# Kernel optimization log

Hardware: AMD Instinct MI355X
Metric: run time of the kernel (lower is better)

## Reference

```python
import jax, jax.numpy as jnp
import numpy as np

BN_EPS = 1e-5
TEMPERATURE = 256 ** 0.5  # sqrt(c2), since cv3 = ScaledDotProductAttention(c2)


def conv_bn_silu(x, w, gamma, beta, mean, var):
    # Conv2d(k=3, s=1, pad='same', bias=False) -> BatchNorm2d (running stats) -> SiLU
    y = jax.lax.conv_general_dilated(
        x, w, window_strides=(1, 1), padding='SAME',
        dimension_numbers=('NCHW', 'OIHW', 'NCHW'))
    scale = (gamma / jnp.sqrt(var + BN_EPS))[None, :, None, None]
    shift = (beta - mean * gamma / jnp.sqrt(var + BN_EPS))[None, :, None, None]
    y = y * scale + shift
    return y * jax.nn.sigmoid(y)  # SiLU


def setup_inputs() -> dict:
    key = jax.random.key(0)
    ks = jax.random.split(key, 8)
    B, C, H, W = 16, 256, 64, 64
    Ch = 128  # hidden channels c_ = int(c2 * e)
    x = jax.random.normal(ks[0], (B, C, H, W), dtype=jnp.float32)
    w1 = jax.random.normal(ks[1], (Ch, C, 3, 3), dtype=jnp.float32) * 0.05
    g1 = jnp.ones((Ch,), jnp.float32) + 0.1 * jax.random.normal(ks[2], (Ch,), dtype=jnp.float32)
    b1 = 0.1 * jax.random.normal(ks[3], (Ch,), dtype=jnp.float32)
    m1 = 0.1 * jax.random.normal(ks[4], (Ch,), dtype=jnp.float32)
    v1 = jnp.ones((Ch,), jnp.float32) + 0.5 * jax.random.uniform(ks[5], (Ch,), dtype=jnp.float32)
    w2 = jax.random.normal(ks[6], (C, Ch, 3, 3), dtype=jnp.float32) * 0.05
    g2 = jnp.ones((C,), jnp.float32)
    b2 = jnp.zeros((C,), jnp.float32)
    m2 = 0.1 * jax.random.normal(ks[7], (C,), dtype=jnp.float32)
    v2 = jnp.ones((C,), jnp.float32) + 0.5 * jax.random.uniform(jax.random.fold_in(key, 99), (C,), dtype=jnp.float32)
    return {"x": x, "w1": w1, "g1": g1, "b1": b1, "m1": m1, "v1": v1,
            "w2": w2, "g2": g2, "b2": b2, "m2": m2, "v2": v2}


def reference(x, w1, g1, b1, m1, v1, w2, g2, b2, m2, v2):
    y = conv_bn_silu(x, w1, g1, b1, m1, v1)       # [B, 128, H, W]
    y = conv_bn_silu(y, w2, g2, b2, m2, v2)       # [B, 256, H, W]
    B, C, H, W = y.shape
    q = y.reshape(B, C, H * W)                    # q = k^T = v, all views of y
    # channel-channel attention: scores [B, C, C]
    scores = jnp.einsum('bcn,bdn->bcd', q / TEMPERATURE, q)
    attn = jax.nn.softmax(scores, axis=-1)        # dropout is identity in eval
    out = jnp.einsum('bcd,bdn->bcn', attn, q).reshape(B, C, H, W)
    return x + out  # shortcut: c1 == c2
```

## Files before the change

kernel.cpp:

```cpp
#include <hip/hip_runtime.h>
#include <math.h>

#define BB 16
#define C1 256
#define CHD 128
#define NN 4096
#define INV_T (1.0f/16.0f)

typedef _Float16 half8 __attribute__((ext_vector_type(8)));
typedef __attribute__((ext_vector_type(4))) float f32x4;
typedef __attribute__((ext_vector_type(16))) float f32x16;

__device__ inline unsigned short f2h(float f) {
    _Float16 h = (_Float16)f;
    return __builtin_bit_cast(unsigned short, h);
}

#define GLDS(g, l) __builtin_amdgcn_global_load_lds(                              \
    (const __attribute__((address_space(1))) unsigned int*)(g),                   \
    (__attribute__((address_space(3))) unsigned int*)(l), 16, 0, 0)

__global__ __launch_bounds__(256) void nchw_to_nhwc_f16(
    const float* __restrict__ x, unsigned short* __restrict__ xh, int C)
{
    const int c0 = blockIdx.x * 64;
    const int hp = blockIdx.y;
    const int b  = blockIdx.z;
    const int nCk = C >> 4;

    if (hp == 0 || hp == 65) {
        for (int idx = threadIdx.x; idx < 1024; idx += 256) {
            int w = idx >> 4, cq = (idx & 15) * 4;
            ushort4 z; z.x = z.y = z.z = z.w = 0;
            *(ushort4*)&xh[((((size_t)b * nCk + (c0 >> 4) + (cq >> 4)) * 66 + hp) * 64 + w) * 16
                           + (cq & 15)] = z;
        }
        return;
    }
    const int h = hp - 1;
    __shared__ float ts[64][65];
    for (int idx = threadIdx.x; idx < 4096; idx += 256) {
        int cl = idx >> 6, w = idx & 63;
        ts[cl][w] = x[(((size_t)b * C + c0 + cl) * 64 + h) * 64 + w];
    }
    __syncthreads();
    for (int idx = threadIdx.x; idx < 1024; idx += 256) {
        int w = idx >> 4, cq = (idx & 15) * 4;
        ushort4 o;
        o.x = f2h(ts[cq + 0][w]); o.y = f2h(ts[cq + 1][w]);
        o.z = f2h(ts[cq + 2][w]); o.w = f2h(ts[cq + 3][w]);
        *(ushort4*)&xh[((((size_t)b * nCk + (c0 >> 4) + (cq >> 4)) * 66 + hp) * 64 + w) * 16
                       + (cq & 15)] = o;
    }
}

__global__ __launch_bounds__(256) void pack_w_kernel(
    const float* __restrict__ w, unsigned short* __restrict__ wT, int Cout, int Cin)
{
    int idx = blockIdx.x * 256 + threadIdx.x;
    int total = Cout * Cin * 9;
    if (idx >= total) return;
    int ci = idx % Cin; int t = idx / Cin; int co = t % Cout; int kk = t / Cout;
    wT[((((size_t)(ci >> 4)) * 9 + kk) * Cout + co) * 16 + (ci & 15)] =
        f2h(w[((size_t)co * Cin + ci) * 9 + kk]);
}

__global__ __launch_bounds__(256) void zero_y1h_pads(unsigned short* __restrict__ y1h)
{
    int idx = blockIdx.x * 256 + threadIdx.x;
    int b   = idx >> 12;
    int ck  = (idx >> 9) & 7;
    int row = ((idx >> 8) & 1) ? 65 : 0;
    int w   = (idx >> 2) & 63;
    int qtr = idx & 3;
    ushort4 z; z.x = z.y = z.z = z.w = 0;
    *(ushort4*)&y1h[((((size_t)b * 8 + ck) * 66 + row) * 64 + w) * 16 + qtr * 4] = z;
}

__global__ __launch_bounds__(512, 4) void conv_mfma_kernel(
    const unsigned short* __restrict__ xh, const unsigned short* __restrict__ wT,
    const float* __restrict__ gamma, const float* __restrict__ beta,
    const float* __restrict__ mean, const float* __restrict__ var,
    unsigned short* __restrict__ outNHWC,
    unsigned short* __restrict__ yhi, unsigned short* __restrict__ yhiT,
    int Cin, int Cout)
{
    const int tid  = threadIdx.x;
    const int wid  = tid >> 6;
    const int lane = tid & 63;
    const int l31  = lane & 31;
    const int hi   = lane >> 5;
    const int coBase = blockIdx.x * 64;
    const int h0     = blockIdx.y * 8;
    const int b      = blockIdx.z;
    const int nCk    = Cin >> 4;

    __shared__ __align__(16) unsigned short smem[39552];
    __shared__ float bnsc[64], bnsh[64];

    if (tid < 64) {
        int co = coBase + tid;
        float sc = gamma[co] * rsqrtf(var[co] + 1e-5f);
        bnsc[tid] = sc;
        bnsh[tid] = beta[co] - mean[co] * sc;
    }
    if (tid < 160) {
        int cell = tid >> 2;
        int part = tid & 3;
        int buf  = cell & 1;
        int col  = ((cell >> 1) & 1) ? 65 : 0;
        int r    = cell >> 2;
        ushort4 z; z.x = z.y = z.z = z.w = 0;
        *(ushort4*)&smem[buf * 10560 + (r * 66 + col) * 16 + part * 4] = z;
    }

    auto stage = [&](int sel, int ck) {
        unsigned short* wsd = smem + 21120 + sel * 9216;
        unsigned short* xsd = smem + sel * 10560;
        for (int it = wid; it < 38; it += 8) {
            if (it < 18) {
                int kk = it >> 1, h = it & 1;
                const unsigned short* g =
                    wT + (((size_t)ck * 9 + kk) * Cout + coBase + h * 32) * 16 + lane * 8;
                GLDS(g, wsd + (kk * 64 + h * 32) * 16);
            } else {
                int j = it - 18;
                int r = j >> 1, hf = j & 1;
                const unsigned short* g =
                    xh + ((((size_t)b * nCk + ck) * 66 + h0 + r) * 64 + hf * 32) * 16 + lane * 8;
                GLDS(g, xsd + (r * 66 + 1 + hf * 32) * 16);
            }
        }
    };

    stage(0, 0);
    __syncthreads();

    f32x16 acc[2][2] = {};

    int sel = 0;
    for (int ck = 0; ck < nCk; ck++) {
        if (ck + 1 < nCk) stage(sel ^ 1, ck + 1);

        const unsigned short* wsb = smem + 21120 + sel * 9216;
        const unsigned short* xsb = smem + sel * 10560;
#pragma unroll
        for (int kk = 0; kk < 9; kk++) {
            const int kh = kk / 3, kw = kk % 3;
            half8 a0 = *(const half8*)&wsb[(kk * 64 +      l31) * 16 + hi * 8];
            half8 a1 = *(const half8*)&wsb[(kk * 64 + 32 + l31) * 16 + hi * 8];
            const unsigned short* xr = &xsb[((wid + kh) * 66 + l31 + kw) * 16 + hi * 8];
            half8 b0 = *(const half8*)xr;
            half8 b1 = *(const half8*)&xr[32 * 16];
            acc[0][0] = __builtin_amdgcn_mfma_f32_32x32x16_f16(a0, b0, acc[0][0], 0, 0, 0);
            acc[0][1] = __builtin_amdgcn_mfma_f32_32x32x16_f16(a0, b1, acc[0][1], 0, 0, 0);
            acc[1][0] = __builtin_amdgcn_mfma_f32_32x32x16_f16(a1, b0, acc[1][0], 0, 0, 0);
            acc[1][1] = __builtin_amdgcn_mfma_f32_32x32x16_f16(a1, b1, acc[1][1], 0, 0, 0);
        }
        __syncthreads();
        sel ^= 1;
    }

    const int orow = h0 + wid;
    const bool isConv1 = (outNHWC != nullptr);

    __syncthreads();

#pragma unroll
    for (int mi = 0; mi < 2; mi++)
#pragma unroll
        for (int ni = 0; ni < 2; ni++) {
            f32x16 a = acc[mi][ni];
            int w = ni * 32 + l31;
            int swz = ((l31 + wid) & 7) << 3;
#pragma unroll
            for (int rq = 0; rq < 4; rq++) {
                int c0 = mi * 32 + rq * 8 + hi * 4;
                ushort4 o; unsigned short* op = (unsigned short*)&o;
#pragma unroll
                for (int r = 0; r < 4; r++) {
                    float t = a[rq * 4 + r] * bnsc[c0 + r] + bnsh[c0 + r];
                    float s = t / (1.f + __expf(-t));
                    op[r] = f2h(s);
                    if (!isConv1)
                        yhi[(((size_t)b * Cout + coBase + c0 + r) * 64 + orow) * 64 + w] = op[r];
                }
                *(ushort4*)&smem[wid * 4096 + w * 64 + (c0 ^ swz)] = o;
            }
        }
    __syncthreads();

    const int ckB = blockIdx.x * 4;
    const int nCkOut = Cout >> 4;
#pragma unroll
    for (int j = 0; j < 8; j++) {
        int g   = j * 512 + tid;
        int s   = g & 1;
        int w   = (g >> 1) & 63;
        int row = (g >> 7) & 7;
        int ck  = g >> 10;
        uint4 v = *(const uint4*)&smem[row * 4096 + w * 64 +
                     (((ck * 2 + s) * 8) ^ (((w + row) & 7) << 3))];
        if (isConv1) {
            *(uint4*)&outNHWC[((((size_t)b * nCkOut + ckB + ck) * 66 + h0 + row + 1) * 64 + w) * 16
                              + s * 8] = v;
        } else {
            *(uint4*)&yhiT[(((size_t)b * nCkOut + ckB + ck) * 4096 + (size_t)(h0 + row) * 64 + w) * 16
                           + s * 8] = v;
        }
    }
}

__global__ __launch_bounds__(256) void scores_mfma_kernel(
    const unsigned short* __restrict__ yhi, float* __restrict__ scores)
{
    static const int TI[10] = {0,0,0,0,1,1,1,2,2,3};
    static const int TJ[10] = {0,1,2,3,1,2,3,2,3,3};
    const int b  = blockIdx.z;
    const int ti = TI[blockIdx.x], tj = TJ[blockIdx.x];
    const int cB = ti * 64;
    const int dB = tj * 64;
    const int tid  = threadIdx.x;
    const int wid  = tid >> 6;
    const int lane = tid & 63;
    const int ln   = lane & 15;
    const int q    = lane >> 4;
    const int wm   = wid >> 1, wn = wid & 1;

    __shared__ unsigned short As[64 * 128];
    __shared__ unsigned short Bs[64 * 128];

    const int rl = lane >> 4;
    const int gl = lane & 15;

    f32x4 acc[2][2] = {};

    for (int ck = 0; ck < 32; ck++) {
        const int n0 = ck * 128;
        for (int it = wid; it < 32; it += 4) {
            const int tile = it >> 4;
            const int j = it & 15;
            const int r = j * 4 + rl;
            const int gq = gl ^ (r & 7);
            const int rowAbs = (tile ? dB : cB) + r;
            const unsigned short* g =
                yhi + ((size_t)b * 256 + rowAbs) * 4096 + n0 + gq * 8;
            GLDS(g, (tile ? Bs : As) + j * 512);
        }
        __syncthreads();

#pragma unroll
        for (int kwin = 0; kwin < 4; kwin++) {
            half8 ah[2], bh[2];
#pragma unroll
            for (int mi = 0; mi < 2; mi++) {
                int row = wm * 32 + mi * 16 + ln;
                ah[mi] = *(const half8*)&As[row * 128 + ((kwin * 4 + q) ^ (ln & 7)) * 8];
            }
#pragma unroll
            for (int ni = 0; ni < 2; ni++) {
                int row = wn * 32 + ni * 16 + ln;
                bh[ni] = *(const half8*)&Bs[row * 128 + ((kwin * 4 + q) ^ (ln & 7)) * 8];
            }
#pragma unroll
            for (int mi = 0; mi < 2; mi++)
#pragma unroll
                for (int ni = 0; ni < 2; ni++)
                    acc[mi][ni] = __builtin_amdgcn_mfma_f32_16x16x32_f16(
                        ah[mi], bh[ni], acc[mi][ni], 0, 0, 0);
        }
        __syncthreads();
    }

#pragma unroll
    for (int mi = 0; mi < 2; mi++)
#pragma unroll
        for (int ni = 0; ni < 2; ni++) {
            f32x4 a = acc[mi][ni];
            float vals[4];
            vals[0] = a.x * INV_T; vals[1] = a.y * INV_T;
            vals[2] = a.z * INV_T; vals[3] = a.w * INV_T;
            int c0 = cB + wm * 32 + mi * 16 + q * 4;
            int d  = dB + wn * 32 + ni * 16 + ln;
#pragma unroll
            for (int r = 0; r < 4; r++)
                scores[((size_t)b * C1 + c0 + r) * C1 + d] = vals[r];
            if (ti != tj) {
                float4 tv = {vals[0], vals[1], vals[2], vals[3]};
                *(float4*)&scores[((size_t)b * C1 + d) * C1 + c0] = tv;
            }
        }
}

__global__ __launch_bounds__(64) void softmax_kernel(
    const float* __restrict__ scores, unsigned short* __restrict__ attn16)
{
    const int row = blockIdx.x;
    const float* p = scores + (size_t)row * C1;
    const int lane = threadIdx.x;

    float4 v = ((const float4*)p)[lane];
    float m = fmaxf(fmaxf(v.x, v.y), fmaxf(v.z, v.w));
#pragma unroll
    for (int off = 32; off >= 1; off >>= 1)
        m = fmaxf(m, __shfl_xor(m, off, 64));

    float4 e;
    e.x = expf(v.x - m); e.y = expf(v.y - m);
    e.z = expf(v.z - m); e.w = expf(v.w - m);
    float s = e.x + e.y + e.z + e.w;
#pragma unroll
    for (int off = 32; off >= 1; off >>= 1)
        s += __shfl_xor(s, off, 64);
    float inv = 1.f / s;
    ushort4 o;
    o.x = f2h(e.x * inv); o.y = f2h(e.y * inv);
    o.z = f2h(e.z * inv); o.w = f2h(e.w * inv);
    *(ushort4*)&attn16[(size_t)row * C1 + lane * 4] = o;
}

__global__ __launch_bounds__(256) void out_mfma_kernel(
    const unsigned short* __restrict__ attn16, const unsigned short* __restrict__ yhiT,
    const float* __restrict__ x, float* __restrict__ out)
{
    const int b  = blockIdx.z;
    const int cB = blockIdx.y * 64;
    const int nB = blockIdx.x * 128;
    const int tid  = threadIdx.x;
    const int wid  = tid >> 6;
    const int lane = tid & 63;
    const int ln   = lane & 15;
    const int q    = lane >> 4;
    const int wm   = wid >> 1, wn = wid & 1;

    __shared__ unsigned short As[64 * 64];
    __shared__ unsigned short Bs[4 * 128 * 16];

    const int r8 = lane >> 3;
    const int gq = (lane & 7) ^ r8;

    f32x4 acc[2][4] = {};

    for (int ck = 0; ck < 4; ck++) {
        const int d0 = ck * 64;
        for (int it = wid; it < 24; it += 4) {
            if (it < 8) {
                const unsigned short* g =
                    attn16 + ((size_t)b * 256 + cB + it * 8 + r8) * 256 + d0 + gq * 8;
                GLDS(g, As + it * 512);
            } else {
                int j = it - 8;
                int u = j >> 2, part = j & 3;
                const unsigned short* g =
                    yhiT + (((size_t)b * 16 + ck * 4 + u) * 4096 + nB + part * 32) * 16 + lane * 8;
                GLDS(g, Bs + (u * 128 + part * 32) * 16);
            }
        }
        __syncthreads();

#pragma unroll
        for (int kwin = 0; kwin < 2; kwin++) {
            const int cc = (((kwin * 4 + q) ^ (ln & 7))) * 8;
            const int gK = kwin * 4 + q;
            half8 af[2], bfr[4];
#pragma unroll
            for (int mi = 0; mi < 2; mi++)
                af[mi] = *(const half8*)&As[(wm * 32 + mi * 16 + ln) * 64 + cc];
#pragma unroll
            for (int ni = 0; ni < 4; ni++) {
                int row = wn * 64 + ni * 16 + ln;
                bfr[ni] = *(const half8*)&Bs[(gK >> 1) * 2048 + row * 16 + (gK & 1) * 8];
            }
#pragma unroll
            for (int mi = 0; mi < 2; mi++)
#pragma unroll
                for (int ni = 0; ni < 4; ni++)
                    acc[mi][ni] = __builtin_amdgcn_mfma_f32_16x16x32_f16(
                        af[mi], bfr[ni], acc[mi][ni], 0, 0, 0);
        }
        __syncthreads();
    }

#pragma unroll
    for (int mi = 0; mi < 2; mi++)
#pragma unroll
        for (int ni = 0; ni < 4; ni++) {
            f32x4 a = acc[mi][ni];
            float vals[4] = {a.x, a.y, a.z, a.w};
#pragma unroll
            for (int r = 0; r < 4; r++) {
                int c = cB + wm * 32 + mi * 16 + q * 4 + r;
                int n = nB + wn * 64 + ni * 16 + ln;
                size_t o = ((size_t)b * C1 + c) * NN + n;
                out[o] = x[o] + vals[r];
            }
        }
}

extern "C" void kernel_launch(void* const* d_in, const int* in_sizes, int n_in,
                              void* d_out, int out_size, void* d_ws, size_t ws_size,
                              hipStream_t stream)
{
    const float* x  = (const float*)d_in[0];
    const float* w1 = (const float*)d_in[1];
    const float* g1 = (const float*)d_in[2];
    const float* b1 = (const float*)d_in[3];
    const float* m1 = (const float*)d_in[4];
    const float* v1 = (const float*)d_in[5];
    const float* w2 = (const float*)d_in[6];
    const float* g2 = (const float*)d_in[7];
    const float* b2 = (const float*)d_in[8];
    const float* m2 = (const float*)d_in[9];
    const float* v2 = (const float*)d_in[10];
    float* out = (float*)d_out;

    unsigned short* xh   = (unsigned short*)d_ws;
    unsigned short* y1h  = xh  + (size_t)17301504;
    unsigned short* wt1  = y1h + (size_t)8650752;
    unsigned short* wt2  = wt1 + (size_t)294912;
    unsigned short* yhiT = wt2 + (size_t)294912;
    unsigned short* yhi  = xh;
    float*          sc   = (float*)y1h;
    unsigned short* attn16 = (unsigned short*)(sc + 1048576);

    nchw_to_nhwc_f16<<<dim3(C1 / 64, 66, BB), 256, 0, stream>>>(x, xh, C1);
    pack_w_kernel<<<(9 * CHD * C1 + 255) / 256, 256, 0, stream>>>(w1, wt1, CHD, C1);
    pack_w_kernel<<<(9 * C1 * CHD + 255) / 256, 256, 0, stream>>>(w2, wt2, C1, CHD);
    zero_y1h_pads<<<256, 256, 0, stream>>>(y1h);

    conv_mfma_kernel<<<dim3(CHD / 64, 8, BB), 512, 0, stream>>>(
        xh, wt1, g1, b1, m1, v1, y1h, nullptr, nullptr, C1, CHD);
    conv_mfma_kernel<<<dim3(C1 / 64, 8, BB), 512, 0, stream>>>(
        y1h, wt2, g2, b2, m2, v2, nullptr, yhi, yhiT, CHD, C1);

    scores_mfma_kernel<<<dim3(10, 1, BB), 256, 0, stream>>>(yhi, sc);
    softmax_kernel<<<dim3(BB * C1), 64, 0, stream>>>(sc, attn16);
    out_mfma_kernel<<<dim3(NN / 128, 4, BB), 256, 0, stream>>>(attn16, yhiT, x, out);
}
```

Before: 326.1 us.

## Split scores reduction over two K halves, remap blocks across XCDs, raise MFMA priority

The scores kernel now splits its N=4096 reduction into two halves along a new grid dimension. Each half writes its own partial score buffer, and the softmax kernel sums the two partials. This doubles the block count from 160 to 320 so more CUs are used. Separately, the conv, scores and output kernels remap block IDs so that consecutive logical tiles land on the same XCD, for L2 locality, and the conv inner MFMA loop raises wave priority. The cost is extra partial-score traffic and one more load in softmax.

```diff
diff --git a/kernel.cpp b/kernel.cpp
--- a/kernel.cpp
+++ b/kernel.cpp
@@ -19,6 +19,14 @@
 #define GLDS(g, l) __builtin_amdgcn_global_load_lds(                              \
     (const __attribute__((address_space(1))) unsigned int*)(g),                   \
     (__attribute__((address_space(3))) unsigned int*)(l), 16, 0, 0)
+
+__device__ inline void xcd_remap(int& bx, int& by, int& bz) {
+    int gx = gridDim.x, gy = gridDim.y;
+    int lin = blockIdx.x + gx * (blockIdx.y + gy * blockIdx.z);
+    int cpx = (gx * gy * (int)gridDim.z) >> 3;
+    lin = (lin & 7) * cpx + (lin >> 3);
+    bx = lin % gx; int t = lin / gx; by = t % gy; bz = t / gy;
+}
 
 __global__ __launch_bounds__(256) void nchw_to_nhwc_f16(
     const float* __restrict__ x, unsigned short* __restrict__ xh, int C)
@@ -85,14 +93,16 @@
     unsigned short* __restrict__ yhi, unsigned short* __restrict__ yhiT,
     int Cin, int Cout)
 {
+    int bx, by, bz;
+    xcd_remap(bx, by, bz);
     const int tid  = threadIdx.x;
     const int wid  = tid >> 6;
     const int lane = tid & 63;
     const int l31  = lane & 31;
     const int hi   = lane >> 5;
-    const int coBase = blockIdx.x * 64;
-    const int h0     = blockIdx.y * 8;
-    const int b      = blockIdx.z;
+    const int coBase = bx * 64;
+    const int h0     = by * 8;
+    const int b      = bz;
     const int nCk    = Cin >> 4;
 
     __shared__ __align__(16) unsigned short smem[39552];
@@ -144,6 +154,7 @@
 
         const unsigned short* wsb = smem + 21120 + sel * 9216;
         const unsigned short* xsb = smem + sel * 10560;
+        __builtin_amdgcn_s_setprio(1);
 #pragma unroll
         for (int kk = 0; kk < 9; kk++) {
             const int kh = kk / 3, kw = kk % 3;
@@ -157,6 +168,7 @@
             acc[1][0] = __builtin_amdgcn_mfma_f32_32x32x16_f16(a1, b0, acc[1][0], 0, 0, 0);
             acc[1][1] = __builtin_amdgcn_mfma_f32_32x32x16_f16(a1, b1, acc[1][1], 0, 0, 0);
         }
+        __builtin_amdgcn_s_setprio(0);
         __syncthreads();
         sel ^= 1;
     }
@@ -190,7 +202,7 @@
         }
     __syncthreads();
 
-    const int ckB = blockIdx.x * 4;
+    const int ckB = bx * 4;
     const int nCkOut = Cout >> 4;
 #pragma unroll
     for (int j = 0; j < 8; j++) {
@@ -216,8 +228,11 @@
 {
     static const int TI[10] = {0,0,0,0,1,1,1,2,2,3};
     static const int TJ[10] = {0,1,2,3,1,2,3,2,3,3};
-    const int b  = blockIdx.z;
-    const int ti = TI[blockIdx.x], tj = TJ[blockIdx.x];
+    int bx, by, bz;
+    xcd_remap(bx, by, bz);
+    const int b  = bz;
+    const int kh = by;
+    const int ti = TI[bx], tj = TJ[bx];
     const int cB = ti * 64;
     const int dB = tj * 64;
     const int tid  = threadIdx.x;
@@ -227,6 +242,8 @@
     const int q    = lane >> 4;
     const int wm   = wid >> 1, wn = wid & 1;
 
+    float* scp = scores + (size_t)kh * 1048576;
+
     __shared__ unsigned short As[64 * 128];
     __shared__ unsigned short Bs[64 * 128];
 
@@ -235,7 +252,7 @@
 
     f32x4 acc[2][2] = {};
 
-    for (int ck = 0; ck < 32; ck++) {
+    for (int ck = kh * 16; ck < kh * 16 + 16; ck++) {
         const int n0 = ck * 128;
         for (int it = wid; it < 32; it += 4) {
             const int tile = it >> 4;
@@ -284,10 +301,10 @@
             int d  = dB + wn * 32 + ni * 16 + ln;
 #pragma unroll
             for (int r = 0; r < 4; r++)
-                scores[((size_t)b * C1 + c0 + r) * C1 + d] = vals[r];
+                scp[((size_t)b * C1 + c0 + r) * C1 + d] = vals[r];
             if (ti != tj) {
                 float4 tv = {vals[0], vals[1], vals[2], vals[3]};
-                *(float4*)&scores[((size_t)b * C1 + d) * C1 + c0] = tv;
+                *(float4*)&scp[((size_t)b * C1 + d) * C1 + c0] = tv;
             }
         }
 }
@@ -299,7 +316,11 @@
     const float* p = scores + (size_t)row * C1;
     const int lane = threadIdx.x;
 
-    float4 v = ((const float4*)p)[lane];
+    float4 v0 = ((const float4*)p)[lane];
+    float4 v1 = ((const float4*)(p + 1048576))[lane];
+    float4 v;
+    v.x = v0.x + v1.x; v.y = v0.y + v1.y;
+    v.z = v0.z + v1.z; v.w = v0.w + v1.w;
     float m = fmaxf(fmaxf(v.x, v.y), fmaxf(v.z, v.w));
 #pragma unroll
     for (int off = 32; off >= 1; off >>= 1)
@@ -323,9 +344,11 @@
     const unsigned short* __restrict__ attn16, const unsigned short* __restrict__ yhiT,
     const float* __restrict__ x, float* __restrict__ out)
 {
-    const int b  = blockIdx.z;
-    const int cB = blockIdx.y * 64;
-    const int nB = blockIdx.x * 128;
+    int bx, by, bz;
+    xcd_remap(bx, by, bz);
+    const int b  = bz;
+    const int cB = by * 64;
+    const int nB = bx * 128;
     const int tid  = threadIdx.x;
     const int wid  = tid >> 6;
     const int lane = tid & 63;
@@ -421,7 +444,7 @@
     unsigned short* yhiT = wt2 + (size_t)294912;
     unsigned short* yhi  = xh;
     float*          sc   = (float*)y1h;
-    unsigned short* attn16 = (unsigned short*)(sc + 1048576);
+    unsigned short* attn16 = (unsigned short*)(sc + 2097152);
 
     nchw_to_nhwc_f16<<<dim3(C1 / 64, 66, BB), 256, 0, stream>>>(x, xh, C1);
     pack_w_kernel<<<(9 * CHD * C1 + 255) / 256, 256, 0, stream>>>(w1, wt1, CHD, C1);
@@ -433,7 +456,7 @@
     conv_mfma_kernel<<<dim3(C1 / 64, 8, BB), 512, 0, stream>>>(
         y1h, wt2, g2, b2, m2, v2, nullptr, yhi, yhiT, CHD, C1);
 
-    scores_mfma_kernel<<<dim3(10, 1, BB), 256, 0, stream>>>(yhi, sc);
+    scores_mfma_kernel<<<dim3(10, 2, BB), 256, 0, stream>>>(yhi, sc);
     softmax_kernel<<<dim3(BB * C1), 64, 0, stream>>>(sc, attn16);
     out_mfma_kernel<<<dim3(NN / 128, 4, BB), 256, 0, stream>>>(attn16, yhiT, x, out);
 }
```

Result: faster. 299.8 us (-8.1%).
